# Performance work log

Measured on AMD Instinct MI355X. Metric: run time of the kernel, lower is better.

Reference implementation:

```python
import jax, jax.numpy as jnp
import numpy as np

# ---- static config (mirrors cfg in torch module) ----
CAM_C = 256
OUT_C = 64
IMG_H, IMG_W = 256, 704
DS = 16
FH, FW = IMG_H // DS, IMG_W // DS  # 16, 44
XB = (-51.2, 51.2, 0.8)
YB = (-51.2, 51.2, 0.8)
ZB = (-10.0, 10.0, 20.0)
DB = (1.0, 60.0, 1.0)
D_BINS = int((DB[1] - DB[0]) / DB[2])  # 59
NX = int((XB[1] - XB[0]) / XB[2])      # 128
NY = int((YB[1] - YB[0]) / YB[2])      # 128
NZ = int((ZB[1] - ZB[0]) / ZB[2])      # 1


def _frustum():
    # [D, FH, FW, 3] of (pixel_x, pixel_y, depth)
    ds = DB[0] + DB[2] * jnp.arange(D_BINS, dtype=jnp.float32)
    ds = jnp.broadcast_to(ds[:, None, None], (D_BINS, FH, FW))
    xs = jnp.broadcast_to(jnp.linspace(0.0, IMG_W - 1, FW, dtype=jnp.float32)[None, None, :], (D_BINS, FH, FW))
    ys = jnp.broadcast_to(jnp.linspace(0.0, IMG_H - 1, FH, dtype=jnp.float32)[None, :, None], (D_BINS, FH, FW))
    return jnp.stack([xs, ys, ds], axis=-1)


def setup_inputs() -> dict:
    key = jax.random.key(0)
    ks = jax.random.split(key, 4)
    B, N = 2, 6
    x = jax.random.normal(ks[0], (B, N, CAM_C, FH, FW), jnp.float32)
    # camera->ego base rotation: ego_x = cam_z, ego_y = -cam_x, ego_z = -cam_y
    base = np.array([[0, 0, 1], [-1, 0, 0], [0, -1, 0]], np.float32)
    rots = np.zeros((B, N, 3, 3), np.float32)
    for i, yaw in enumerate(np.linspace(0.0, 2 * np.pi, N, endpoint=False)):
        c, s = np.cos(yaw), np.sin(yaw)
        Rz = np.array([[c, -s, 0], [s, c, 0], [0, 0, 1]], np.float32)
        rots[:, i] = Rz @ base
    trans = np.asarray(jax.random.normal(ks[1], (B, N, 3)), np.float32) * 1.5
    K = np.array([[400.0, 0.0, IMG_W / 2.0], [0.0, 400.0, IMG_H / 2.0], [0.0, 0.0, 1.0]], np.float32)
    intrins = np.broadcast_to(K, (B, N, 3, 3)).copy()
    depth_w = jax.random.normal(ks[2], (D_BINS + OUT_C, CAM_C, 1, 1), jnp.float32) * 0.02
    depth_b = jnp.zeros((D_BINS + OUT_C,), jnp.float32)
    return dict(x=x, rots=jnp.asarray(rots), trans=jnp.asarray(trans),
                intrins=jnp.asarray(intrins), depth_w=depth_w, depth_b=depth_b)


def reference(x, rots, trans, intrins, depth_w, depth_b):
    B, N = x.shape[0], x.shape[1]
    # depth_net: 1x1 conv == channel matmul
    w = depth_w[:, :, 0, 0]  # [D+C, CAM_C]
    feat = jnp.einsum('bnchw,oc->bnohw', x, w) + depth_b[None, None, :, None, None]
    depth = jax.nn.softmax(feat[:, :, :D_BINS], axis=2)        # [B,N,D,FH,FW]
    ctx = feat[:, :, D_BINS:]                                  # [B,N,C,FH,FW]
    # lift: outer product context x depth  -> [B,N,D,FH,FW,C]
    outer = ctx[:, :, :, None] * depth[:, :, None]             # [B,N,C,D,FH,FW]
    outer = jnp.transpose(outer, (0, 1, 3, 4, 5, 2))

    # geometry: unproject frustum to ego frame
    fr = _frustum()
    pts = jnp.concatenate([fr[..., :2] * fr[..., 2:3], fr[..., 2:3]], axis=-1)  # [D,FH,FW,3]
    comb = rots @ jnp.linalg.inv(intrins)                      # [B,N,3,3]
    geom = jnp.einsum('bnij,dhwj->bndhwi', comb, pts) + trans[:, :, None, None, None, :]

    # voxelize
    dx = jnp.array([XB[2], YB[2], ZB[2]], jnp.float32)
    bx = jnp.array([XB[0] + XB[2] / 2.0, YB[0] + YB[2] / 2.0, ZB[0] + ZB[2] / 2.0], jnp.float32)
    coords = jnp.floor((geom - (bx - dx / 2.0)) / dx).astype(jnp.int32)  # [B,N,D,FH,FW,3]

    Np = B * N * D_BINS * FH * FW
    coords = coords.reshape(Np, 3)
    feats = outer.reshape(Np, OUT_C)
    kept = ((coords[:, 0] >= 0) & (coords[:, 0] < NX) &
            (coords[:, 1] >= 0) & (coords[:, 1] < NY) &
            (coords[:, 2] >= 0) & (coords[:, 2] < NZ))
    batch_ix = jnp.repeat(jnp.arange(B, dtype=jnp.int32), N * D_BINS * FH * FW)
    ranks = batch_ix * (NX * NY * NZ) + coords[:, 0] + coords[:, 1] * NX + coords[:, 2] * (NX * NY)
    ranks = jnp.where(kept, ranks, 0)                 # out-of-grid -> dummy seg 0 with zero feats
    feats = feats * kept[:, None].astype(feats.dtype)
    # sort+cumsum-diff+scatter in the original == segment sum over voxel ranks
    flat = jax.ops.segment_sum(feats, ranks, num_segments=B * NZ * NY * NX)  # [B*nz*ny*nx, C]
    bev = flat.reshape(B, NZ, NY, NX, OUT_C)
    bev = jnp.transpose(bev, (0, 4, 1, 2, 3)).sum(axis=2)  # [B, C, NY, NX]
    return bev


if __name__ == '__main__':
    out = reference(**setup_inputs())
    print(out.shape, out.dtype)
```

## Files before the change

### kernel.cpp

```cpp
#include <hip/hip_runtime.h>
#include <hip/hip_bf16.h>
#include <math.h>

#define B_   2
#define N_   6
#define CC   256
#define OCH  64
#define DBN  59
#define FH_  16
#define FW_  44
#define PXI  (FH_*FW_)
#define NPIX (B_*N_*PXI)
#define NPTS (B_*N_*DBN*PXI)
#define NX_  128
#define NY_  128
#define NCELL (B_*NY_*NX_)
#define NOUT 123
#define OUTSZ (B_*OCH*NY_*NX_)
#define TCH  32

#define XSTEP (703.0f/43.0f)
#define YSTEP (255.0f/15.0f)

__device__ __forceinline__ void comb_cam(const float* __restrict__ R,
                                         const float* __restrict__ K,
                                         float* __restrict__ out9) {
    float a = K[0], b = K[1], c = K[2];
    float d = K[3], e = K[4], f = K[5];
    float g = K[6], h = K[7], k = K[8];
    float A  =  __fsub_rn(__fmul_rn(e, k), __fmul_rn(f, h));
    float Bc = -__fsub_rn(__fmul_rn(d, k), __fmul_rn(f, g));
    float Cc =  __fsub_rn(__fmul_rn(d, h), __fmul_rn(e, g));
    float det = __fadd_rn(__fadd_rn(__fmul_rn(a, A), __fmul_rn(b, Bc)),
                          __fmul_rn(c, Cc));
    float inv[9];
    inv[0] = __fdiv_rn(A, det);
    inv[1] = __fdiv_rn(-__fsub_rn(__fmul_rn(b, k), __fmul_rn(c, h)), det);
    inv[2] = __fdiv_rn( __fsub_rn(__fmul_rn(b, f), __fmul_rn(c, e)), det);
    inv[3] = __fdiv_rn(Bc, det);
    inv[4] = __fdiv_rn( __fsub_rn(__fmul_rn(a, k), __fmul_rn(c, g)), det);
    inv[5] = __fdiv_rn(-__fsub_rn(__fmul_rn(a, f), __fmul_rn(c, d)), det);
    inv[6] = __fdiv_rn(Cc, det);
    inv[7] = __fdiv_rn(-__fsub_rn(__fmul_rn(a, h), __fmul_rn(b, g)), det);
    inv[8] = __fdiv_rn( __fsub_rn(__fmul_rn(a, e), __fmul_rn(b, d)), det);
    for (int r = 0; r < 3; ++r)
        for (int cc = 0; cc < 3; ++cc) {
            float s =        __fmul_rn(R[r*3+0], inv[0*3+cc]);
            s = __fadd_rn(s, __fmul_rn(R[r*3+1], inv[1*3+cc]));
            s = __fadd_rn(s, __fmul_rn(R[r*3+2], inv[2*3+cc]));
            out9[r*3 + cc] = s;
        }
}

template <int NK>
__global__ __launch_bounds__(256) void k_conv_split(
        const float* __restrict__ x, const float* __restrict__ wgt,
        float* __restrict__ parts, unsigned* __restrict__ cellofs) {
    constexpr int KC = CC / NK;
    __shared__ float xs[KC * 64];
    const int t = threadIdx.x;
    const int gid = blockIdx.x * 256 + t;
    const int stride = gridDim.x * 256;
    for (int i = gid; i < NCELL; i += stride) cellofs[i] = 0u;

    const int kc   = blockIdx.x % NK;
    const int half = (blockIdx.x / NK) & 1;
    const int pg   = blockIdx.x / (2 * NK);
    const int pix0 = pg * 64;
    const int bn = pix0 / PXI;
    const int q0 = pix0 - bn * PXI;
    const float* xb = x + (size_t)bn * CC * PXI + (size_t)(kc * KC) * PXI + q0;

    {
        const int p0 = (t & 15) * 4;
        const int cbase = t >> 4;
        #pragma unroll
        for (int r = 0; r < KC / 16; ++r) {
            const int c = r * 16 + cbase;
            const float4 v = *(const float4*)(xb + (size_t)c * PXI + p0);
            *(float4*)&xs[c * 64 + p0] = v;
        }
    }
    __syncthreads();

    const int w = t >> 6;
    const int lane = t & 63;
    const int o0 = __builtin_amdgcn_readfirstlane(half * 62 + w * 16);
    const int lim = half ? NOUT : 62;

    const float* wp[16];
    #pragma unroll
    for (int kk = 0; kk < 16; ++kk) {
        int oc = o0 + kk; if (oc > NOUT - 1) oc = NOUT - 1;
        wp[kk] = wgt + (size_t)oc * CC + kc * KC;
    }
    float acc[16];
    #pragma unroll
    for (int kk = 0; kk < 16; ++kk) acc[kk] = 0.f;

    #pragma unroll 4
    for (int c = 0; c < KC; ++c) {
        const float xv = xs[c * 64 + lane];
        #pragma unroll
        for (int kk = 0; kk < 16; ++kk)
            acc[kk] = fmaf(xv, wp[kk][c], acc[kk]);
    }

    #pragma unroll
    for (int kk = 0; kk < 16; ++kk) {
        const int o = o0 + kk;
        if (o >= lim) break;
        parts[((size_t)kc * NOUT + o) * NPIX + pix0 + lane] = acc[kk];
    }
}

template <int NK>
__global__ __launch_bounds__(256) void k_reduce(
        const float* __restrict__ parts, const float* __restrict__ bias,
        float* __restrict__ dlog, float* __restrict__ ctx_ws,
        float2* __restrict__ msum) {
    __shared__ float lds[NOUT * 65];
    const int t = threadIdx.x;
    const int w = t >> 6;
    const int lane = t & 63;
    const int pix0 = blockIdx.x * 64;

    #pragma unroll
    for (int j = 0; j < 31; ++j) {
        const int o = w * 31 + j;
        if (o >= NOUT) break;
        float s = parts[(size_t)o * NPIX + pix0 + lane];
        #pragma unroll
        for (int k = 1; k < NK; ++k)
            s += parts[((size_t)k * NOUT + o) * NPIX + pix0 + lane];
        s += bias[o];
        lds[o * 65 + lane] = s;
        if (o < DBN) dlog[(size_t)o * NPIX + pix0 + lane] = s;
    }
    __syncthreads();

    if (t < 64) {
        float m = -1e30f;
        #pragma unroll
        for (int d = 0; d < DBN; ++d) m = fmaxf(m, lds[d * 65 + t]);
        float s = 0.f;
        #pragma unroll
        for (int d = 0; d < DBN; ++d) s += expf(lds[d * 65 + t] - m);
        msum[pix0 + t] = make_float2(m, 1.0f / s);
    }

    const int ch = t & 63;
    const int pq = t >> 6;
    #pragma unroll
    for (int px = pq; px < 64; px += 4)
        ctx_ws[(size_t)(pix0 + px) * OCH + ch] = lds[(DBN + ch) * 65 + px];
}

__global__ __launch_bounds__(256) void k_conv_mono(
        const float* __restrict__ x, const float* __restrict__ wgt,
        const float* __restrict__ bias,
        float* __restrict__ dlog, float* __restrict__ ctx_ws,
        float2* __restrict__ msum, unsigned* __restrict__ cellofs) {
    __shared__ float xs[CC * 64];
    const int t = threadIdx.x;
    const int gid = blockIdx.x * 256 + t;
    const int stride = gridDim.x * 256;
    for (int i = gid; i < NCELL; i += stride) cellofs[i] = 0u;

    const int pg = blockIdx.x >> 1;
    const int half = blockIdx.x & 1;
    const int pix0 = pg * 64;
    const int bn = pix0 / PXI;
    const int q0 = pix0 - bn * PXI;
    const float* xb = x + (size_t)bn * CC * PXI + q0;

    {
        const int p0 = (t & 15) * 4;
        const int cbase = t >> 4;
        #pragma unroll
        for (int r = 0; r < 16; ++r) {
            const int c = r * 16 + cbase;
            const float4 v = *(const float4*)(xb + (size_t)c * PXI + p0);
            *(float4*)&xs[c * 64 + p0] = v;
        }
    }
    __syncthreads();

    const int w = t >> 6;
    const int lane = t & 63;
    const int o0 = __builtin_amdgcn_readfirstlane(half * 62 + w * 16);
    const int lim = half ? NOUT : 62;

    const float* wp[16];
    #pragma unroll
    for (int kk = 0; kk < 16; ++kk) {
        int oc = o0 + kk; if (oc > NOUT - 1) oc = NOUT - 1;
        wp[kk] = wgt + (size_t)oc * CC;
    }
    float acc[16];
    #pragma unroll
    for (int kk = 0; kk < 16; ++kk) acc[kk] = 0.f;

    #pragma unroll 4
    for (int c = 0; c < CC; ++c) {
        const float xv = xs[c * 64 + lane];
        #pragma unroll
        for (int kk = 0; kk < 16; ++kk)
            acc[kk] = fmaf(xv, wp[kk][c], acc[kk]);
    }

    float av[16];
    #pragma unroll
    for (int kk = 0; kk < 16; ++kk) {
        const int o = o0 + kk;
        if (o >= lim) break;
        const float a = acc[kk] + bias[o];
        av[kk] = a;
        if (o < DBN) dlog[(size_t)o * NPIX + pix0 + lane] = a;
        else         ctx_ws[(size_t)(pix0 + lane) * OCH + (o - DBN)] = a;
    }

    __syncthreads();
    if (half == 0) {
        #pragma unroll
        for (int kk = 0; kk < 16; ++kk) {
            const int o = o0 + kk;
            if (o >= lim) break;
            if (o < DBN) xs[o * 64 + lane] = av[kk];
        }
    }
    __syncthreads();
    if (half == 0 && t < 64) {
        float m = -1e30f;
        #pragma unroll
        for (int d = 0; d < DBN; ++d) m = fmaxf(m, xs[d * 64 + t]);
        float s = 0.f;
        #pragma unroll
        for (int d = 0; d < DBN; ++d) s += expf(xs[d * 64 + t] - m);
        msum[pix0 + t] = make_float2(m, 1.0f / s);
    }
}

__global__ __launch_bounds__(256) void k_geom(
        const float* __restrict__ rots, const float* __restrict__ intrins,
        const float* __restrict__ trans,
        unsigned short* __restrict__ cell16, unsigned* __restrict__ cellofs) {
    __shared__ float combs[B_ * N_ * 9];
    __shared__ float trs[B_ * N_ * 3];
    const int t = threadIdx.x;
    if (t < B_ * N_) comb_cam(rots + t * 9, intrins + t * 9, &combs[t * 9]);
    if (t < B_ * N_ * 3) trs[t] = trans[t];
    __syncthreads();

    const int pt = blockIdx.x * 256 + t;
    const int q  = pt % PXI;
    const int r  = pt / PXI;
    const int dq = r % DBN;
    const int bn = r / DBN;
    const int hq = q / FW_;
    const int wq = q - hq * FW_;
    const int bq = bn / N_;

    const float* cb = &combs[bn * 9];
    const float t0 = trs[bn*3+0], t1 = trs[bn*3+1], t2 = trs[bn*3+2];

    const float dsv = __fadd_rn(1.0f, (float)dq);
    const float xsv = __fmul_rn((float)wq, XSTEP);
    const float ysv = __fmul_rn((float)hq, YSTEP);
    const float px = __fmul_rn(xsv, dsv);
    const float py = __fmul_rn(ysv, dsv);
    const float pz = dsv;
    float gx = __fadd_rn(__fadd_rn(__fmul_rn(cb[0], px), __fmul_rn(cb[1], py)),
                         __fmul_rn(cb[2], pz));
    float gy = __fadd_rn(__fadd_rn(__fmul_rn(cb[3], px), __fmul_rn(cb[4], py)),
                         __fmul_rn(cb[5], pz));
    float gz = __fadd_rn(__fadd_rn(__fmul_rn(cb[6], px), __fmul_rn(cb[7], py)),
                         __fmul_rn(cb[8], pz));
    gx = __fadd_rn(gx, t0);
    gy = __fadd_rn(gy, t1);
    gz = __fadd_rn(gz, t2);

    const float bxv = -50.8f;
    const float lbx = __fsub_rn(bxv, 0.4f);
    const float lbz = -10.0f;
    const int cx = (int)floorf(__fdiv_rn(__fsub_rn(gx, lbx), 0.8f));
    const int cy = (int)floorf(__fdiv_rn(__fsub_rn(gy, lbx), 0.8f));
    const int cz = (int)floorf(__fdiv_rn(__fsub_rn(gz, lbz), 20.0f));

    int c = -1;
    if (cx >= 0 && cx < NX_ && cy >= 0 && cy < NY_ && cz == 0)
        c = bq * (NY_ * NX_) + cy * NX_ + cx;
    cell16[pt] = (c >= 0) ? (unsigned short)c : (unsigned short)0xFFFFu;

    const int lane = t & 63;
    unsigned long long active = __ballot(c >= 0);
    while (active) {
        const int leader = (int)__ffsll((unsigned long long)active) - 1;
        const int lc = __shfl(c, leader);
        const unsigned long long same = __ballot(c == lc);
        if (lane == leader)
            atomicAdd(&cellofs[lc], (unsigned)__popcll(same));
        active &= ~same;
    }
}

__global__ __launch_bounds__(1024) void k_scan(unsigned* __restrict__ cellofs) {
    __shared__ unsigned lds[2][1024];
    const int t = threadIdx.x;
    uint4 u[8];
    const uint4* src4 = (const uint4*)cellofs + (size_t)t * 8;
    #pragma unroll
    for (int i = 0; i < 8; ++i) u[i] = src4[i];
    unsigned vv[32];
    unsigned run = 0;
    #pragma unroll
    for (int i = 0; i < 8; ++i) {
        vv[i*4+0] = run; run += u[i].x;
        vv[i*4+1] = run; run += u[i].y;
        vv[i*4+2] = run; run += u[i].z;
        vv[i*4+3] = run; run += u[i].w;
    }
    lds[0][t] = run;
    __syncthreads();
    int src = 0;
    for (int off = 1; off < 1024; off <<= 1) {
        unsigned val = lds[src][t];
        if (t >= off) val += lds[src][t - off];
        lds[1 - src][t] = val;
        __syncthreads();
        src = 1 - src;
    }
    const unsigned base = (t == 0) ? 0u : lds[src][t - 1];
    uint4* dst4 = (uint4*)cellofs + (size_t)t * 8;
    #pragma unroll
    for (int i = 0; i < 8; ++i) {
        uint4 w;
        w.x = base + vv[i*4+0];
        w.y = base + vv[i*4+1];
        w.z = base + vv[i*4+2];
        w.w = base + vv[i*4+3];
        dst4[i] = w;
    }
}

__global__ __launch_bounds__(256) void k_fill(
        const unsigned short* __restrict__ cell16,
        const float* __restrict__ dlog, const float2* __restrict__ msum,
        unsigned* __restrict__ cellofs, uint2* __restrict__ srt) {
    const int pt = blockIdx.x * 256 + threadIdx.x;
    const unsigned cc = cell16[pt];
    const int c = (cc == 0xFFFFu) ? -1 : (int)cc;
    const int lane = threadIdx.x & 63;

    unsigned slot = 0;
    unsigned long long active = __ballot(c >= 0);
    while (active) {
        const int leader = (int)__ffsll((unsigned long long)active) - 1;
        const int lc = __shfl(c, leader);
        const unsigned long long same = __ballot(c == lc);
        unsigned b0 = 0;
        if (lane == leader)
            b0 = atomicAdd(&cellofs[lc], (unsigned)__popcll(same));
        b0 = __shfl(b0, leader);
        if (c == lc)
            slot = b0 + (unsigned)__popcll(same & ((1ULL << lane) - 1ULL));
        active &= ~same;
    }

    if (c >= 0) {
        const int q  = pt % PXI;
        const int r  = pt / PXI;
        const int dq = r % DBN;
        const int bn = r / DBN;
        const int pix = bn * PXI + q;
        const float2 ms = msum[pix];
        const float w = expf(dlog[(size_t)dq * NPIX + pix] - ms.x) * ms.y;
        srt[slot] = make_uint2(((unsigned)c << 14) | (unsigned)pix,
                               __float_as_uint(w));
    }
}

__device__ __forceinline__ void flush_cell(float* __restrict__ tmp, unsigned cell,
                                           int ch, float acc, bool use_atomic) {
    float* dst = &tmp[((size_t)cell << 6) + ch];
    if (use_atomic) atomicAdd(dst, acc);
    else            *dst = acc;
}

__global__ __launch_bounds__(256) void k_gather(
        const unsigned* __restrict__ cellofs, const uint2* __restrict__ srt,
        const float* __restrict__ ctx_ws, float* __restrict__ tmp) {
    const int wid = __builtin_amdgcn_readfirstlane(
                        (blockIdx.x * 256 + threadIdx.x) >> 6);
    const int ch = threadIdx.x & 63;
    const unsigned K = cellofs[NCELL - 1];
    unsigned i = (unsigned)wid * TCH;
    if (i >= K) return;
    const unsigned s1 = (i + TCH < K) ? (i + TCH) : K;

    unsigned cur = srt[i].x >> 14;
    float acc = 0.f;
    bool flushed = false;

    while (i + 8 <= s1) {
        uint2 r8[8]; float v8[8];
        #pragma unroll
        for (int j = 0; j < 8; ++j) r8[j] = srt[i + j];
        #pragma unroll
        for (int j = 0; j < 8; ++j)
            v8[j] = ctx_ws[(size_t)(r8[j].x & 0x3FFFu) * OCH + ch];
        #pragma unroll
        for (int j = 0; j < 8; ++j) {
            const unsigned c = r8[j].x >> 14;
            if (c != cur) {
                flush_cell(tmp, cur, ch, acc, !flushed);
                flushed = true;
                acc = 0.f;
                cur = c;
            }
            acc = fmaf(__uint_as_float(r8[j].y), v8[j], acc);
        }
        i += 8;
    }
    while (i < s1) {
        const uint2 rr = srt[i];
        const float vv = ctx_ws[(size_t)(rr.x & 0x3FFFu) * OCH + ch];
        const unsigned c = rr.x >> 14;
        if (c != cur) {
            flush_cell(tmp, cur, ch, acc, !flushed);
            flushed = true;
            acc = 0.f;
            cur = c;
        }
        acc = fmaf(__uint_as_float(rr.y), vv, acc);
        ++i;
    }
    flush_cell(tmp, cur, ch, acc, true);
}

__global__ __launch_bounds__(256) void k_transpose(
        const float* __restrict__ tmp, float* __restrict__ out) {
    __shared__ float tile[64 * 65];
    const int t = threadIdx.x;
    const int w = t >> 6;
    const int lane = t & 63;
    const int b = blockIdx.x >> 8;
    const int c0 = (blockIdx.x & 255) * 64;

    #pragma unroll
    for (int r = 0; r < 16; ++r) {
        const int row = r * 4 + w;
        const float v = tmp[((size_t)(b * (NY_ * NX_) + c0 + row) << 6) + lane];
        tile[lane * 65 + row] = v;
    }
    __syncthreads();
    #pragma unroll
    for (int r = 0; r < 16; ++r) {
        const int chv = r * 4 + w;
        out[((size_t)(b * OCH + chv) * (NY_ * NX_)) + c0 + lane] =
            tile[chv * 65 + lane];
    }
}

extern "C" void kernel_launch(void* const* d_in, const int* in_sizes, int n_in,
                              void* d_out, int out_size, void* d_ws, size_t ws_size,
                              hipStream_t stream) {
    const float* x       = (const float*)d_in[0];
    const float* rots    = (const float*)d_in[1];
    const float* trans   = (const float*)d_in[2];
    const float* intrins = (const float*)d_in[3];
    const float* depth_w = (const float*)d_in[4];
    const float* depth_b = (const float*)d_in[5];
    float* out = (float*)d_out;
    float* ws = (float*)d_ws;

    float* tmp      = ws;
    float* dlog     = ws;
    unsigned short* cell16 = (unsigned short*)(ws + 524288);
    float2* msum    = (float2*)(ws + 786432);
    float* ctx_ws   = ws + 2097152;
    unsigned* cellofs = (unsigned*)(ws + 2637824);
    uint2* srt      = (uint2*)(ws + 2670592);
    float* parts    = ws + 3667456;

    const size_t BASE = 14669824;
    const size_t PART1 = (size_t)NOUT * NPIX * 4;
    const int gblocks = (NPTS / TCH + 3) / 4;

    if (ws_size >= BASE + 4 * PART1) {
        k_conv_split<4><<<132 * 2 * 4, 256, 0, stream>>>(x, depth_w,
                                                         parts, cellofs);
        k_reduce<4><<<132, 256, 0, stream>>>(parts, depth_b, dlog, ctx_ws,
                                             msum);
    } else if (ws_size >= BASE + 2 * PART1) {
        k_conv_split<2><<<132 * 2 * 2, 256, 0, stream>>>(x, depth_w,
                                                         parts, cellofs);
        k_reduce<2><<<132, 256, 0, stream>>>(parts, depth_b, dlog, ctx_ws,
                                             msum);
    } else {
        k_conv_mono<<<264, 256, 0, stream>>>(x, depth_w, depth_b, dlog,
                                             ctx_ws, msum, cellofs);
    }

    k_geom<<<NPTS / 256, 256, 0, stream>>>(rots, intrins, trans,
                                           cell16, cellofs);
    k_scan<<<1, 1024, 0, stream>>>(cellofs);
    k_fill<<<NPTS / 256, 256, 0, stream>>>(cell16, dlog, msum, cellofs, srt);
    hipMemsetAsync(tmp, 0, (size_t)NCELL * OCH * sizeof(float), stream);
    k_gather<<<gblocks, 256, 0, stream>>>(cellofs, srt, ctx_ws, tmp);
    k_transpose<<<512, 256, 0, stream>>>(tmp, out);
}
```

Measured before the change: 175.3 us.

## Merge conv-split with geometry, scan with reduce, and fold tmp zeroing into fill

Geometry and voxel-count blocks now run in the same launch as the split-K depth conv, so the two independent stages share the GPU. The prefix scan becomes block 0 of the partial-sum reduce kernel, and zeroing of the BEV accumulator moves into the fill kernel instead of a separate memset. A separate memset for cellofs is added. The aim is fewer launches and better use of the GPU in the small stages. The risks are that one block serially scans 32K cells while the other blocks reduce, and the workspace gets a new, larger layout with a fallback path.

```diff
diff --git a/kernel.cpp b/kernel.cpp
--- a/kernel.cpp
+++ b/kernel.cpp
@@ -18,6 +18,7 @@
 #define NOUT 123
 #define OUTSZ (B_*OCH*NY_*NX_)
 #define TCH  32
+#define NK_  4
 
 #define XSTEP (703.0f/43.0f)
 #define YSTEP (255.0f/15.0f)
@@ -52,207 +53,8 @@
         }
 }
 
-template <int NK>
-__global__ __launch_bounds__(256) void k_conv_split(
-        const float* __restrict__ x, const float* __restrict__ wgt,
-        float* __restrict__ parts, unsigned* __restrict__ cellofs) {
-    constexpr int KC = CC / NK;
-    __shared__ float xs[KC * 64];
-    const int t = threadIdx.x;
-    const int gid = blockIdx.x * 256 + t;
-    const int stride = gridDim.x * 256;
-    for (int i = gid; i < NCELL; i += stride) cellofs[i] = 0u;
-
-    const int kc   = blockIdx.x % NK;
-    const int half = (blockIdx.x / NK) & 1;
-    const int pg   = blockIdx.x / (2 * NK);
-    const int pix0 = pg * 64;
-    const int bn = pix0 / PXI;
-    const int q0 = pix0 - bn * PXI;
-    const float* xb = x + (size_t)bn * CC * PXI + (size_t)(kc * KC) * PXI + q0;
-
-    {
-        const int p0 = (t & 15) * 4;
-        const int cbase = t >> 4;
-        #pragma unroll
-        for (int r = 0; r < KC / 16; ++r) {
-            const int c = r * 16 + cbase;
-            const float4 v = *(const float4*)(xb + (size_t)c * PXI + p0);
-            *(float4*)&xs[c * 64 + p0] = v;
-        }
-    }
-    __syncthreads();
-
-    const int w = t >> 6;
-    const int lane = t & 63;
-    const int o0 = __builtin_amdgcn_readfirstlane(half * 62 + w * 16);
-    const int lim = half ? NOUT : 62;
-
-    const float* wp[16];
-    #pragma unroll
-    for (int kk = 0; kk < 16; ++kk) {
-        int oc = o0 + kk; if (oc > NOUT - 1) oc = NOUT - 1;
-        wp[kk] = wgt + (size_t)oc * CC + kc * KC;
-    }
-    float acc[16];
-    #pragma unroll
-    for (int kk = 0; kk < 16; ++kk) acc[kk] = 0.f;
-
-    #pragma unroll 4
-    for (int c = 0; c < KC; ++c) {
-        const float xv = xs[c * 64 + lane];
-        #pragma unroll
-        for (int kk = 0; kk < 16; ++kk)
-            acc[kk] = fmaf(xv, wp[kk][c], acc[kk]);
-    }
-
-    #pragma unroll
-    for (int kk = 0; kk < 16; ++kk) {
-        const int o = o0 + kk;
-        if (o >= lim) break;
-        parts[((size_t)kc * NOUT + o) * NPIX + pix0 + lane] = acc[kk];
-    }
-}
-
-template <int NK>
-__global__ __launch_bounds__(256) void k_reduce(
-        const float* __restrict__ parts, const float* __restrict__ bias,
-        float* __restrict__ dlog, float* __restrict__ ctx_ws,
-        float2* __restrict__ msum) {
-    __shared__ float lds[NOUT * 65];
-    const int t = threadIdx.x;
-    const int w = t >> 6;
-    const int lane = t & 63;
-    const int pix0 = blockIdx.x * 64;
-
-    #pragma unroll
-    for (int j = 0; j < 31; ++j) {
-        const int o = w * 31 + j;
-        if (o >= NOUT) break;
-        float s = parts[(size_t)o * NPIX + pix0 + lane];
-        #pragma unroll
-        for (int k = 1; k < NK; ++k)
-            s += parts[((size_t)k * NOUT + o) * NPIX + pix0 + lane];
-        s += bias[o];
-        lds[o * 65 + lane] = s;
-        if (o < DBN) dlog[(size_t)o * NPIX + pix0 + lane] = s;
-    }
-    __syncthreads();
-
-    if (t < 64) {
-        float m = -1e30f;
-        #pragma unroll
-        for (int d = 0; d < DBN; ++d) m = fmaxf(m, lds[d * 65 + t]);
-        float s = 0.f;
-        #pragma unroll
-        for (int d = 0; d < DBN; ++d) s += expf(lds[d * 65 + t] - m);
-        msum[pix0 + t] = make_float2(m, 1.0f / s);
-    }
-
-    const int ch = t & 63;
-    const int pq = t >> 6;
-    #pragma unroll
-    for (int px = pq; px < 64; px += 4)
-        ctx_ws[(size_t)(pix0 + px) * OCH + ch] = lds[(DBN + ch) * 65 + px];
-}
-
-__global__ __launch_bounds__(256) void k_conv_mono(
-        const float* __restrict__ x, const float* __restrict__ wgt,
-        const float* __restrict__ bias,
-        float* __restrict__ dlog, float* __restrict__ ctx_ws,
-        float2* __restrict__ msum, unsigned* __restrict__ cellofs) {
-    __shared__ float xs[CC * 64];
-    const int t = threadIdx.x;
-    const int gid = blockIdx.x * 256 + t;
-    const int stride = gridDim.x * 256;
-    for (int i = gid; i < NCELL; i += stride) cellofs[i] = 0u;
-
-    const int pg = blockIdx.x >> 1;
-    const int half = blockIdx.x & 1;
-    const int pix0 = pg * 64;
-    const int bn = pix0 / PXI;
-    const int q0 = pix0 - bn * PXI;
-    const float* xb = x + (size_t)bn * CC * PXI + q0;
-
-    {
-        const int p0 = (t & 15) * 4;
-        const int cbase = t >> 4;
-        #pragma unroll
-        for (int r = 0; r < 16; ++r) {
-            const int c = r * 16 + cbase;
-            const float4 v = *(const float4*)(xb + (size_t)c * PXI + p0);
-            *(float4*)&xs[c * 64 + p0] = v;
-        }
-    }
-    __syncthreads();
-
-    const int w = t >> 6;
-    const int lane = t & 63;
-    const int o0 = __builtin_amdgcn_readfirstlane(half * 62 + w * 16);
-    const int lim = half ? NOUT : 62;
-
-    const float* wp[16];
-    #pragma unroll
-    for (int kk = 0; kk < 16; ++kk) {
-        int oc = o0 + kk; if (oc > NOUT - 1) oc = NOUT - 1;
-        wp[kk] = wgt + (size_t)oc * CC;
-    }
-    float acc[16];
-    #pragma unroll
-    for (int kk = 0; kk < 16; ++kk) acc[kk] = 0.f;
-
-    #pragma unroll 4
-    for (int c = 0; c < CC; ++c) {
-        const float xv = xs[c * 64 + lane];
-        #pragma unroll
-        for (int kk = 0; kk < 16; ++kk)
-            acc[kk] = fmaf(xv, wp[kk][c], acc[kk]);
-    }
-
-    float av[16];
-    #pragma unroll
-    for (int kk = 0; kk < 16; ++kk) {
-        const int o = o0 + kk;
-        if (o >= lim) break;
-        const float a = acc[kk] + bias[o];
-        av[kk] = a;
-        if (o < DBN) dlog[(size_t)o * NPIX + pix0 + lane] = a;
-        else         ctx_ws[(size_t)(pix0 + lane) * OCH + (o - DBN)] = a;
-    }
-
-    __syncthreads();
-    if (half == 0) {
-        #pragma unroll
-        for (int kk = 0; kk < 16; ++kk) {
-            const int o = o0 + kk;
-            if (o >= lim) break;
-            if (o < DBN) xs[o * 64 + lane] = av[kk];
-        }
-    }
-    __syncthreads();
-    if (half == 0 && t < 64) {
-        float m = -1e30f;
-        #pragma unroll
-        for (int d = 0; d < DBN; ++d) m = fmaxf(m, xs[d * 64 + t]);
-        float s = 0.f;
-        #pragma unroll
-        for (int d = 0; d < DBN; ++d) s += expf(xs[d * 64 + t] - m);
-        msum[pix0 + t] = make_float2(m, 1.0f / s);
-    }
-}
-
-__global__ __launch_bounds__(256) void k_geom(
-        const float* __restrict__ rots, const float* __restrict__ intrins,
-        const float* __restrict__ trans,
-        unsigned short* __restrict__ cell16, unsigned* __restrict__ cellofs) {
-    __shared__ float combs[B_ * N_ * 9];
-    __shared__ float trs[B_ * N_ * 3];
-    const int t = threadIdx.x;
-    if (t < B_ * N_) comb_cam(rots + t * 9, intrins + t * 9, &combs[t * 9]);
-    if (t < B_ * N_ * 3) trs[t] = trans[t];
-    __syncthreads();
-
-    const int pt = blockIdx.x * 256 + t;
+__device__ __forceinline__ int geom_cell(int pt, const float* __restrict__ combs,
+                                         const float* __restrict__ trs) {
     const int q  = pt % PXI;
     const int r  = pt / PXI;
     const int dq = r % DBN;
@@ -287,67 +89,185 @@
     const int cy = (int)floorf(__fdiv_rn(__fsub_rn(gy, lbx), 0.8f));
     const int cz = (int)floorf(__fdiv_rn(__fsub_rn(gz, lbz), 20.0f));
 
-    int c = -1;
     if (cx >= 0 && cx < NX_ && cy >= 0 && cy < NY_ && cz == 0)
-        c = bq * (NY_ * NX_) + cy * NX_ + cx;
-    cell16[pt] = (c >= 0) ? (unsigned short)c : (unsigned short)0xFFFFu;
-
-    const int lane = t & 63;
-    unsigned long long active = __ballot(c >= 0);
-    while (active) {
-        const int leader = (int)__ffsll((unsigned long long)active) - 1;
-        const int lc = __shfl(c, leader);
-        const unsigned long long same = __ballot(c == lc);
-        if (lane == leader)
-            atomicAdd(&cellofs[lc], (unsigned)__popcll(same));
-        active &= ~same;
-    }
-}
-
-__global__ __launch_bounds__(1024) void k_scan(unsigned* __restrict__ cellofs) {
-    __shared__ unsigned lds[2][1024];
+        return bq * (NY_ * NX_) + cy * NX_ + cx;
+    return -1;
+}
+
+template <int NK>
+__global__ __launch_bounds__(256) void k_front(
+        const float* __restrict__ x, const float* __restrict__ wgt,
+        const float* __restrict__ rots, const float* __restrict__ intrins,
+        const float* __restrict__ trans,
+        float* __restrict__ parts, unsigned short* __restrict__ cell16,
+        unsigned* __restrict__ cellofs) {
+    constexpr int KC = CC / NK;
+    constexpr int NCONV = 132 * 2 * NK;
+    __shared__ float xs[KC * 64];
+    __shared__ float combs[B_ * N_ * 9];
+    __shared__ float trs[B_ * N_ * 3];
     const int t = threadIdx.x;
-    uint4 u[8];
-    const uint4* src4 = (const uint4*)cellofs + (size_t)t * 8;
-    #pragma unroll
-    for (int i = 0; i < 8; ++i) u[i] = src4[i];
-    unsigned vv[32];
-    unsigned run = 0;
-    #pragma unroll
-    for (int i = 0; i < 8; ++i) {
-        vv[i*4+0] = run; run += u[i].x;
-        vv[i*4+1] = run; run += u[i].y;
-        vv[i*4+2] = run; run += u[i].z;
-        vv[i*4+3] = run; run += u[i].w;
-    }
-    lds[0][t] = run;
-    __syncthreads();
-    int src = 0;
-    for (int off = 1; off < 1024; off <<= 1) {
-        unsigned val = lds[src][t];
-        if (t >= off) val += lds[src][t - off];
-        lds[1 - src][t] = val;
+
+    if (blockIdx.x < NCONV) {
+        const int kc   = blockIdx.x % NK;
+        const int half = (blockIdx.x / NK) & 1;
+        const int pg   = blockIdx.x / (2 * NK);
+        const int pix0 = pg * 64;
+        const int bn = pix0 / PXI;
+        const int q0 = pix0 - bn * PXI;
+        const float* xb = x + (size_t)bn * CC * PXI
+                            + (size_t)(kc * KC) * PXI + q0;
+        {
+            const int p0 = (t & 15) * 4;
+            const int cbase = t >> 4;
+            #pragma unroll
+            for (int r = 0; r < KC / 16; ++r) {
+                const int c = r * 16 + cbase;
+                const float4 v = *(const float4*)(xb + (size_t)c * PXI + p0);
+                *(float4*)&xs[c * 64 + p0] = v;
+            }
+        }
         __syncthreads();
-        src = 1 - src;
-    }
-    const unsigned base = (t == 0) ? 0u : lds[src][t - 1];
-    uint4* dst4 = (uint4*)cellofs + (size_t)t * 8;
-    #pragma unroll
-    for (int i = 0; i < 8; ++i) {
-        uint4 w;
-        w.x = base + vv[i*4+0];
-        w.y = base + vv[i*4+1];
-        w.z = base + vv[i*4+2];
-        w.w = base + vv[i*4+3];
-        dst4[i] = w;
+
+        const int w = t >> 6;
+        const int lane = t & 63;
+        const int o0 = __builtin_amdgcn_readfirstlane(half * 62 + w * 16);
+        const int lim = half ? NOUT : 62;
+
+        const float* wp[16];
+        #pragma unroll
+        for (int kk = 0; kk < 16; ++kk) {
+            int oc = o0 + kk; if (oc > NOUT - 1) oc = NOUT - 1;
+            wp[kk] = wgt + (size_t)oc * CC + kc * KC;
+        }
+        float acc[16];
+        #pragma unroll
+        for (int kk = 0; kk < 16; ++kk) acc[kk] = 0.f;
+
+        #pragma unroll 4
+        for (int c = 0; c < KC; ++c) {
+            const float xv = xs[c * 64 + lane];
+            #pragma unroll
+            for (int kk = 0; kk < 16; ++kk)
+                acc[kk] = fmaf(xv, wp[kk][c], acc[kk]);
+        }
+        #pragma unroll
+        for (int kk = 0; kk < 16; ++kk) {
+            const int o = o0 + kk;
+            if (o >= lim) break;
+            parts[((size_t)kc * NOUT + o) * NPIX + pix0 + lane] = acc[kk];
+        }
+    } else {
+        if (t < B_ * N_) comb_cam(rots + t * 9, intrins + t * 9, &combs[t * 9]);
+        if (t < B_ * N_ * 3) trs[t] = trans[t];
+        __syncthreads();
+
+        const int pt = (blockIdx.x - NCONV) * 256 + t;
+        const int c = geom_cell(pt, combs, trs);
+        cell16[pt] = (c >= 0) ? (unsigned short)c : (unsigned short)0xFFFFu;
+
+        const int lane = t & 63;
+        unsigned long long active = __ballot(c >= 0);
+        while (active) {
+            const int leader = (int)__ffsll((unsigned long long)active) - 1;
+            const int lc = __shfl(c, leader);
+            const unsigned long long same = __ballot(c == lc);
+            if (lane == leader)
+                atomicAdd(&cellofs[lc], (unsigned)__popcll(same));
+            active &= ~same;
+        }
+    }
+}
+
+template <int NK>
+__global__ __launch_bounds__(256) void k_mid(
+        const float* __restrict__ parts, const float* __restrict__ bias,
+        unsigned* __restrict__ cellofs,
+        float* __restrict__ dlog, float* __restrict__ ctx_ws,
+        float2* __restrict__ msum) {
+    __shared__ float lds[NOUT * 65];
+    __shared__ unsigned sc[2][256];
+    const int t = threadIdx.x;
+
+    if (blockIdx.x == 0) {
+        const uint4* s4 = (const uint4*)cellofs + (size_t)t * 32;
+        unsigned run = 0;
+        #pragma unroll 8
+        for (int i = 0; i < 32; ++i) {
+            const uint4 v = s4[i];
+            run += v.x + v.y + v.z + v.w;
+        }
+        sc[0][t] = run;
+        __syncthreads();
+        int src = 0;
+        for (int off = 1; off < 256; off <<= 1) {
+            unsigned val = sc[src][t];
+            if (t >= off) val += sc[src][t - off];
+            sc[1 - src][t] = val;
+            __syncthreads();
+            src = 1 - src;
+        }
+        unsigned base = (t == 0) ? 0u : sc[src][t - 1];
+        uint4* d4 = (uint4*)cellofs + (size_t)t * 32;
+        #pragma unroll 8
+        for (int i = 0; i < 32; ++i) {
+            const uint4 v = d4[i];
+            uint4 w;
+            w.x = base; base += v.x;
+            w.y = base; base += v.y;
+            w.z = base; base += v.z;
+            w.w = base; base += v.w;
+            d4[i] = w;
+        }
+    } else {
+        const int w = t >> 6;
+        const int lane = t & 63;
+        const int pix0 = (blockIdx.x - 1) * 64;
+
+        #pragma unroll
+        for (int j = 0; j < 31; ++j) {
+            const int o = w * 31 + j;
+            if (o >= NOUT) break;
+            float s = parts[(size_t)o * NPIX + pix0 + lane];
+            #pragma unroll
+            for (int k = 1; k < NK; ++k)
+                s += parts[((size_t)k * NOUT + o) * NPIX + pix0 + lane];
+            s += bias[o];
+            lds[o * 65 + lane] = s;
+            if (o < DBN) dlog[(size_t)o * NPIX + pix0 + lane] = s;
+        }
+        __syncthreads();
+
+        if (t < 64) {
+            float m = -1e30f;
+            #pragma unroll
+            for (int d = 0; d < DBN; ++d) m = fmaxf(m, lds[d * 65 + t]);
+            float s = 0.f;
+            #pragma unroll
+            for (int d = 0; d < DBN; ++d) s += expf(lds[d * 65 + t] - m);
+            msum[pix0 + t] = make_float2(m, 1.0f / s);
+        }
+        const int ch = t & 63;
+        const int pq = t >> 6;
+        #pragma unroll
+        for (int px = pq; px < 64; px += 4)
+            ctx_ws[(size_t)(pix0 + px) * OCH + ch] = lds[(DBN + ch) * 65 + px];
     }
 }
 
 __global__ __launch_bounds__(256) void k_fill(
         const unsigned short* __restrict__ cell16,
         const float* __restrict__ dlog, const float2* __restrict__ msum,
-        unsigned* __restrict__ cellofs, uint2* __restrict__ srt) {
-    const int pt = blockIdx.x * 256 + threadIdx.x;
+        unsigned* __restrict__ cellofs, uint2* __restrict__ srt,
+        float4* __restrict__ tmpz) {
+    const int gid = blockIdx.x * 256 + threadIdx.x;
+    if (tmpz) {
+        const int stride = (NPTS / 256) * 256;
+        for (int i = gid; i < OUTSZ / 4; i += stride)
+            tmpz[i] = make_float4(0.f, 0.f, 0.f, 0.f);
+    }
+
+    const int pt = gid;
     const unsigned cc = cell16[pt];
     const int c = (cc == 0xFFFFu) ? -1 : (int)cc;
     const int lane = threadIdx.x & 63;
@@ -462,6 +382,157 @@
     }
 }
 
+__global__ __launch_bounds__(256) void k_conv_mono(
+        const float* __restrict__ x, const float* __restrict__ wgt,
+        const float* __restrict__ bias,
+        float* __restrict__ dlog, float* __restrict__ ctx_ws,
+        float2* __restrict__ msum, unsigned* __restrict__ cellofs) {
+    __shared__ float xs[CC * 64];
+    const int t = threadIdx.x;
+    const int gid = blockIdx.x * 256 + t;
+    const int stride = gridDim.x * 256;
+    for (int i = gid; i < NCELL; i += stride) cellofs[i] = 0u;
+
+    const int pg = blockIdx.x >> 1;
+    const int half = blockIdx.x & 1;
+    const int pix0 = pg * 64;
+    const int bn = pix0 / PXI;
+    const int q0 = pix0 - bn * PXI;
+    const float* xb = x + (size_t)bn * CC * PXI + q0;
+
+    {
+        const int p0 = (t & 15) * 4;
+        const int cbase = t >> 4;
+        #pragma unroll
+        for (int r = 0; r < 16; ++r) {
+            const int c = r * 16 + cbase;
+            const float4 v = *(const float4*)(xb + (size_t)c * PXI + p0);
+            *(float4*)&xs[c * 64 + p0] = v;
+        }
+    }
+    __syncthreads();
+
+    const int w = t >> 6;
+    const int lane = t & 63;
+    const int o0 = __builtin_amdgcn_readfirstlane(half * 62 + w * 16);
+    const int lim = half ? NOUT : 62;
+
+    const float* wp[16];
+    #pragma unroll
+    for (int kk = 0; kk < 16; ++kk) {
+        int oc = o0 + kk; if (oc > NOUT - 1) oc = NOUT - 1;
+        wp[kk] = wgt + (size_t)oc * CC;
+    }
+    float acc[16];
+    #pragma unroll
+    for (int kk = 0; kk < 16; ++kk) acc[kk] = 0.f;
+
+    #pragma unroll 4
+    for (int c = 0; c < CC; ++c) {
+        const float xv = xs[c * 64 + lane];
+        #pragma unroll
+        for (int kk = 0; kk < 16; ++kk)
+            acc[kk] = fmaf(xv, wp[kk][c], acc[kk]);
+    }
+
+    float av[16];
+    #pragma unroll
+    for (int kk = 0; kk < 16; ++kk) {
+        const int o = o0 + kk;
+        if (o >= lim) break;
+        const float a = acc[kk] + bias[o];
+        av[kk] = a;
+        if (o < DBN) dlog[(size_t)o * NPIX + pix0 + lane] = a;
+        else         ctx_ws[(size_t)(pix0 + lane) * OCH + (o - DBN)] = a;
+    }
+
+    __syncthreads();
+    if (half == 0) {
+        #pragma unroll
+        for (int kk = 0; kk < 16; ++kk) {
+            const int o = o0 + kk;
+            if (o >= lim) break;
+            if (o < DBN) xs[o * 64 + lane] = av[kk];
+        }
+    }
+    __syncthreads();
+    if (half == 0 && t < 64) {
+        float m = -1e30f;
+        #pragma unroll
+        for (int d = 0; d < DBN; ++d) m = fmaxf(m, xs[d * 64 + t]);
+        float s = 0.f;
+        #pragma unroll
+        for (int d = 0; d < DBN; ++d) s += expf(xs[d * 64 + t] - m);
+        msum[pix0 + t] = make_float2(m, 1.0f / s);
+    }
+}
+
+__global__ __launch_bounds__(256) void k_geom_only(
+        const float* __restrict__ rots, const float* __restrict__ intrins,
+        const float* __restrict__ trans,
+        unsigned short* __restrict__ cell16, unsigned* __restrict__ cellofs) {
+    __shared__ float combs[B_ * N_ * 9];
+    __shared__ float trs[B_ * N_ * 3];
+    const int t = threadIdx.x;
+    if (t < B_ * N_) comb_cam(rots + t * 9, intrins + t * 9, &combs[t * 9]);
+    if (t < B_ * N_ * 3) trs[t] = trans[t];
+    __syncthreads();
+
+    const int pt = blockIdx.x * 256 + t;
+    const int c = geom_cell(pt, combs, trs);
+    cell16[pt] = (c >= 0) ? (unsigned short)c : (unsigned short)0xFFFFu;
+
+    const int lane = t & 63;
+    unsigned long long active = __ballot(c >= 0);
+    while (active) {
+        const int leader = (int)__ffsll((unsigned long long)active) - 1;
+        const int lc = __shfl(c, leader);
+        const unsigned long long same = __ballot(c == lc);
+        if (lane == leader)
+            atomicAdd(&cellofs[lc], (unsigned)__popcll(same));
+        active &= ~same;
+    }
+}
+
+__global__ __launch_bounds__(1024) void k_scan1024(unsigned* __restrict__ cellofs) {
+    __shared__ unsigned lds[2][1024];
+    const int t = threadIdx.x;
+    uint4 u[8];
+    const uint4* src4 = (const uint4*)cellofs + (size_t)t * 8;
+    #pragma unroll
+    for (int i = 0; i < 8; ++i) u[i] = src4[i];
+    unsigned vv[32];
+    unsigned run = 0;
+    #pragma unroll
+    for (int i = 0; i < 8; ++i) {
+        vv[i*4+0] = run; run += u[i].x;
+        vv[i*4+1] = run; run += u[i].y;
+        vv[i*4+2] = run; run += u[i].z;
+        vv[i*4+3] = run; run += u[i].w;
+    }
+    lds[0][t] = run;
+    __syncthreads();
+    int src = 0;
+    for (int off = 1; off < 1024; off <<= 1) {
+        unsigned val = lds[src][t];
+        if (t >= off) val += lds[src][t - off];
+        lds[1 - src][t] = val;
+        __syncthreads();
+        src = 1 - src;
+    }
+    const unsigned base = (t == 0) ? 0u : lds[src][t - 1];
+    uint4* dst4 = (uint4*)cellofs + (size_t)t * 8;
+    #pragma unroll
+    for (int i = 0; i < 8; ++i) {
+        uint4 w;
+        w.x = base + vv[i*4+0];
+        w.y = base + vv[i*4+1];
+        w.z = base + vv[i*4+2];
+        w.w = base + vv[i*4+3];
+        dst4[i] = w;
+    }
+}
+
 extern "C" void kernel_launch(void* const* d_in, const int* in_sizes, int n_in,
                               void* d_out, int out_size, void* d_ws, size_t ws_size,
                               hipStream_t stream) {
@@ -472,41 +543,47 @@
     const float* depth_w = (const float*)d_in[4];
     const float* depth_b = (const float*)d_in[5];
     float* out = (float*)d_out;
-    float* ws = (float*)d_ws;
-
-    float* tmp      = ws;
-    float* dlog     = ws;
-    unsigned short* cell16 = (unsigned short*)(ws + 524288);
-    float2* msum    = (float2*)(ws + 786432);
-    float* ctx_ws   = ws + 2097152;
-    unsigned* cellofs = (unsigned*)(ws + 2637824);
-    uint2* srt      = (uint2*)(ws + 2670592);
-    float* parts    = ws + 3667456;
-
-    const size_t BASE = 14669824;
-    const size_t PART1 = (size_t)NOUT * NPIX * 4;
+    char* ws = (char*)d_ws;
+
     const int gblocks = (NPTS / TCH + 3) / 4;
 
-    if (ws_size >= BASE + 4 * PART1) {
-        k_conv_split<4><<<132 * 2 * 4, 256, 0, stream>>>(x, depth_w,
-                                                         parts, cellofs);
-        k_reduce<4><<<132, 256, 0, stream>>>(parts, depth_b, dlog, ctx_ws,
-                                             msum);
-    } else if (ws_size >= BASE + 2 * PART1) {
-        k_conv_split<2><<<132 * 2 * 2, 256, 0, stream>>>(x, depth_w,
-                                                         parts, cellofs);
-        k_reduce<2><<<132, 256, 0, stream>>>(parts, depth_b, dlog, ctx_ws,
-                                             msum);
+    if (ws_size >= 34353664) {
+        float*    dlog    = (float*)   (ws + 0);
+        float2*   msum    = (float2*)  (ws + 1993728);
+        unsigned* cellofs = (unsigned*)(ws + 2061312);
+        unsigned short* cell16 = (unsigned short*)(ws + 2192384);
+        float*    ctx_ws  = (float*)   (ws + 3189248);
+        uint2*    srt     = (uint2*)   (ws + 5351936);
+        float*    parts   = (float*)   (ws + 9339392);
+        float*    tmp     = (float*)   (ws + 25965056);
+
+        hipMemsetAsync(cellofs, 0, NCELL * sizeof(unsigned), stream);
+        k_front<NK_><<<132 * 2 * NK_ + NPTS / 256, 256, 0, stream>>>(
+            x, depth_w, rots, intrins, trans, parts, cell16, cellofs);
+        k_mid<NK_><<<133, 256, 0, stream>>>(parts, depth_b, cellofs,
+                                            dlog, ctx_ws, msum);
+        k_fill<<<NPTS / 256, 256, 0, stream>>>(cell16, dlog, msum, cellofs,
+                                               srt, (float4*)tmp);
+        k_gather<<<gblocks, 256, 0, stream>>>(cellofs, srt, ctx_ws, tmp);
+        k_transpose<<<512, 256, 0, stream>>>(tmp, out);
     } else {
+        float* tmp      = (float*)(ws);
+        float* dlog     = (float*)(ws);
+        unsigned short* cell16 = (unsigned short*)(ws + 2097152);
+        float2* msum    = (float2*)(ws + 3145728);
+        float* ctx_ws   = (float*)(ws + 8388608);
+        unsigned* cellofs = (unsigned*)(ws + 10551296);
+        uint2* srt      = (uint2*)(ws + 10682368);
+
         k_conv_mono<<<264, 256, 0, stream>>>(x, depth_w, depth_b, dlog,
                                              ctx_ws, msum, cellofs);
-    }
-
-    k_geom<<<NPTS / 256, 256, 0, stream>>>(rots, intrins, trans,
-                                           cell16, cellofs);
-    k_scan<<<1, 1024, 0, stream>>>(cellofs);
-    k_fill<<<NPTS / 256, 256, 0, stream>>>(cell16, dlog, msum, cellofs, srt);
-    hipMemsetAsync(tmp, 0, (size_t)NCELL * OCH * sizeof(float), stream);
-    k_gather<<<gblocks, 256, 0, stream>>>(cellofs, srt, ctx_ws, tmp);
-    k_transpose<<<512, 256, 0, stream>>>(tmp, out);
-}
+        k_geom_only<<<NPTS / 256, 256, 0, stream>>>(rots, intrins, trans,
+                                                    cell16, cellofs);
+        k_scan1024<<<1, 1024, 0, stream>>>(cellofs);
+        k_fill<<<NPTS / 256, 256, 0, stream>>>(cell16, dlog, msum, cellofs,
+                                               srt, nullptr);
+        hipMemsetAsync(tmp, 0, (size_t)NCELL * OCH * sizeof(float), stream);
+        k_gather<<<gblocks, 256, 0, stream>>>(cellofs, srt, ctx_ws, tmp);
+        k_transpose<<<512, 256, 0, stream>>>(tmp, out);
+    }
+}
```

Result: faster. 152.7 us (-12.8%).
